# Performance work log

Measured on AMD Instinct MI355X. Metric: run time of the kernel, lower is better.

Reference implementation:

```python
import jax, jax.numpy as jnp
import numpy as np

NUM_EXPERT = 16
IN_FEAT = 1024
OUT_FEAT = 1024
BATCH = 8192


def setup_inputs() -> dict:
    key = jax.random.key(0)
    k_inp, k_gate, k_w = jax.random.split(key, 3)
    inp = jax.random.normal(k_inp, (BATCH, IN_FEAT), dtype=jnp.float32)
    gate = jax.random.randint(k_gate, (BATCH,), 0, NUM_EXPERT, dtype=jnp.int32)
    # nn.Linear default init: uniform(-1/sqrt(in_feat), 1/sqrt(in_feat))
    bound = 1.0 / np.sqrt(IN_FEAT)
    weight = jax.random.uniform(
        k_w, (NUM_EXPERT, OUT_FEAT, IN_FEAT), dtype=jnp.float32,
        minval=-bound, maxval=bound)
    return {"inp": inp, "gate": gate, "weight": weight}


def reference(inp, gate, weight):
    # o[t] = weight[gate[t]] @ inp[t]
    # Loop over the (small, fixed) expert axis via lax.scan; each step does a
    # dense [B, in] @ [in, out] GEMM and keeps rows routed to that expert.
    num_expert, out_feat, _ = weight.shape
    batch = inp.shape[0]

    def body(o, xs):
        i, w = xs  # w: [out_feat, in_feat]
        y = inp @ w.T  # [batch, out_feat]
        sel = (gate == i)[:, None]
        return jnp.where(sel, y, o), None

    o0 = jnp.zeros((batch, out_feat), dtype=inp.dtype)
    o, _ = jax.lax.scan(body, o0, (jnp.arange(num_expert), weight))
    return o
```

## Files before the change

kernel.cpp:

```cpp
#include <hip/hip_runtime.h>
#include <hip/hip_bf16.h>

#define NE    16
#define KDIM  1024
#define NDIM  1024
#define BATCH 8192
#define TM    128
#define TN    64
#define MAXT  96

typedef __attribute__((ext_vector_type(8))) short short8;
typedef __attribute__((ext_vector_type(4))) float floatx4;
typedef unsigned short ushort_t;

#define O_CNT  0
#define O_OFF  64
#define O_TG0  256
#define O_TE   1024
#define O_TEND 2048
#define O_POS  4096
#define O_TOK  36864
#define O_PA   73728
#define O_W    17113088
#define WS_REQ 50667520

#define GLOAD_LDS(gp, lp) __builtin_amdgcn_global_load_lds( \
    (const __attribute__((address_space(1))) unsigned int*)(gp), \
    (__attribute__((address_space(3))) unsigned int*)(lp), 16, 0, 0)

__device__ __forceinline__ unsigned int pk2bf(float x, float y) {
    __hip_bfloat162 h = __float22bfloat162_rn(make_float2(x, y));
    unsigned int u;
    __builtin_memcpy(&u, &h, 4);
    return u;
}


__global__ void zero_k(int* cnt) {
    if (threadIdx.x < NE) cnt[threadIdx.x] = 0;
}

__global__ void hist_k(const int* __restrict__ gate, int* cnt, int* pos) {
    int t = blockIdx.x * blockDim.x + threadIdx.x;
    if (t < BATCH) pos[t] = atomicAdd(&cnt[gate[t]], 1);
}

__global__ void scan_k(const int* __restrict__ cnt, int* off,
                       int* tg0, int* te, int* tend) {
    __shared__ int ntot;
    int t = threadIdx.x;
    if (t < NE) {
        int o = 0, ts = 0;
        for (int j = 0; j < NE; ++j) {
            int c = cnt[j];
            if (j < t) { o += c; ts += (c + TM - 1) / TM; }
        }
        int c = cnt[t];
        off[t] = o;
        if (t == NE - 1) { off[NE] = o + c; ntot = ts + (c + TM - 1) / TM; }
        int nt = ts;
        for (int r = 0; r < c; r += TM) {
            int r0 = (r + TM <= c) ? r : (c > TM ? c - TM : 0);
            tg0[nt] = o + r0; te[nt] = t; tend[nt] = o + c; ++nt;
        }
    }
    __syncthreads();
    for (int i = ntot + t; i < MAXT; i += 64) {
        tg0[i] = 0; te[i] = 0; tend[i] = 0;
    }
}

__global__ __launch_bounds__(256) void prep_k(
        const float* __restrict__ inp, const float* __restrict__ wgt,
        const int* __restrict__ gate, const int* __restrict__ pos,
        const int* __restrict__ off, ushort_t* __restrict__ pA,
        ushort_t* __restrict__ pW, int* __restrict__ tok) {
    int b = blockIdx.x, tid = threadIdx.x;
    if (b < BATCH) {
        int t = b;
        int g = off[gate[t]] + pos[t];
        float4 v = *(const float4*)&inp[(size_t)t * KDIM + tid * 4];
        uint2 u = make_uint2(pk2bf(v.x, v.y), pk2bf(v.z, v.w));
        *(uint2*)&pA[(size_t)g * KDIM + tid * 4] = u;
        if (tid == 0) tok[g] = t;
    } else {
        size_t i = (size_t)(b - BATCH) * 1024 + tid * 4;
        float4 v = *(const float4*)&wgt[i];
        uint2 u = make_uint2(pk2bf(v.x, v.y), pk2bf(v.z, v.w));
        *(uint2*)&pW[i] = u;
    }
}

__global__ __launch_bounds__(256, 4) void moe_gemm3_k(
        const ushort_t* __restrict__ pA, const ushort_t* __restrict__ pW,
        const int* __restrict__ tg0, const int* __restrict__ teArr,
        const int* __restrict__ tend, const int* __restrict__ tok,
        float* __restrict__ out) {
    const int y   = blockIdx.y;
    const int g0  = tg0[y];
    const int end = tend[y];
    if (g0 >= end) return;
    const int e    = teArr[y];
    const int out0 = blockIdx.x * TN;

    __shared__ ushort_t As[2][TM][32];
    __shared__ ushort_t Bs[2][TN][32];
    __shared__ int tok_s[TM];

    const int tid = threadIdx.x;
    if (tid < TM) tok_s[tid] = tok[g0 + tid];

    const int wave = tid >> 6, lane = tid & 63;
    const int wm = (wave >> 1) * 64;
    const int wn = (wave & 1) * 32;
    const int quad = lane >> 4, l16 = lane & 15;

    const ushort_t* Ab = pA + (size_t)g0 * KDIM;
    const ushort_t* Bb = pW + (size_t)e * (KDIM * NDIM) + (size_t)out0 * KDIM;

    floatx4 acc[4][2] = {};

    const int cA0 = wave * 64 + lane;
    const int cB  = wave * 64 + lane;

    {
        #pragma unroll
        for (int i = 0; i < 2; ++i) {
            int c = cA0 + i * 256;
            GLOAD_LDS(Ab + (c >> 2) * KDIM + (c & 3) * 8,
                      (ushort_t*)As[0] + (size_t)(i * 256 + wave * 64) * 8);
        }
        GLOAD_LDS(Bb + (cB >> 2) * KDIM + (cB & 3) * 8,
                  (ushort_t*)Bs[0] + (size_t)(wave * 64) * 8);
    }

    int buf = 0;
    for (int k0 = 0; k0 < KDIM; k0 += 32, buf ^= 1) {
        __syncthreads();
        if (k0 + 32 < KDIM) {
            int kn = k0 + 32;
            #pragma unroll
            for (int i = 0; i < 2; ++i) {
                int c = cA0 + i * 256;
                GLOAD_LDS(Ab + (c >> 2) * KDIM + kn + (c & 3) * 8,
                          (ushort_t*)As[buf ^ 1] + (size_t)(i * 256 + wave * 64) * 8);
            }
            GLOAD_LDS(Bb + (cB >> 2) * KDIM + kn + (cB & 3) * 8,
                      (ushort_t*)Bs[buf ^ 1] + (size_t)(wave * 64) * 8);
        }
        short8 a[4], b[2];
        #pragma unroll
        for (int i = 0; i < 4; ++i)
            a[i] = *(const short8*)&As[buf][wm + i * 16 + l16][quad * 8];
        #pragma unroll
        for (int i = 0; i < 2; ++i)
            b[i] = *(const short8*)&Bs[buf][wn + i * 16 + l16][quad * 8];
        #pragma unroll
        for (int mi = 0; mi < 4; ++mi)
            #pragma unroll
            for (int ni = 0; ni < 2; ++ni)
                acc[mi][ni] = __builtin_amdgcn_mfma_f32_16x16x32_bf16(
                    a[mi], b[ni], acc[mi][ni], 0, 0, 0);
    }

    #pragma unroll
    for (int mi = 0; mi < 4; ++mi) {
        #pragma unroll
        for (int r = 0; r < 4; ++r) {
            int lrow = wm + mi * 16 + quad * 4 + r;
            if (g0 + lrow < end) {
                int t = tok_s[lrow];
                float* orow = out + (size_t)t * NDIM + out0 + wn + l16;
                #pragma unroll
                for (int ni = 0; ni < 2; ++ni)
                    orow[ni * 16] = acc[mi][ni][r];
            }
        }
    }
}

#define LDW 20
__global__ void bin_tokens_k(const int* __restrict__ gate, int* cnt, int* idx) {
    int t = blockIdx.x * blockDim.x + threadIdx.x;
    if (t < BATCH) {
        int e = gate[t];
        int p = atomicAdd(&cnt[e], 1);
        idx[e * BATCH + p] = t;
    }
}

__global__ __launch_bounds__(256) void moe_gemm_k(
        const float* __restrict__ inp, const float* __restrict__ wgt,
        const int* __restrict__ cnt, const int* __restrict__ idx,
        float* __restrict__ out) {
    const int e = blockIdx.z;
    const int n_e = cnt[e];
    const int row0 = blockIdx.y * TM;
    if (row0 >= n_e) return;
    const int out0 = blockIdx.x * 128;
    __shared__ unsigned int As[TM * LDW];
    __shared__ unsigned int Bs[TM * LDW];
    __shared__ int tok_s[TM];
    const int tid = threadIdx.x;
    if (tid < TM) {
        int g = row0 + tid;
        tok_s[tid] = (g < n_e) ? idx[e * BATCH + g] : -1;
    }
    const int wave = tid >> 6, lane = tid & 63;
    const int wm = (wave >> 1) * 64, wn = (wave & 1) * 64;
    const int quad = lane >> 4, l16 = lane & 15;
    floatx4 acc[4][4] = {};
    const int cg = (tid & 7) * 4;
    const int rbase = tid >> 3;
    const float* wbase = wgt + (size_t)e * KDIM * NDIM;
    for (int k0 = 0; k0 < KDIM; k0 += 32) {
        __syncthreads();
        #pragma unroll
        for (int p = 0; p < 4; ++p) {
            int row = p * 32 + rbase;
            int t = tok_s[row];
            float4 va = make_float4(0.f, 0.f, 0.f, 0.f);
            if (t >= 0) va = *(const float4*)&inp[(size_t)t * KDIM + k0 + cg];
            As[row * LDW + (cg >> 1)]     = pk2bf(va.x, va.y);
            As[row * LDW + (cg >> 1) + 1] = pk2bf(va.z, va.w);
            float4 vb = *(const float4*)&wbase[(size_t)(out0 + row) * KDIM + k0 + cg];
            Bs[row * LDW + (cg >> 1)]     = pk2bf(vb.x, vb.y);
            Bs[row * LDW + (cg >> 1) + 1] = pk2bf(vb.z, vb.w);
        }
        __syncthreads();
        short8 a[4], b[4];
        #pragma unroll
        for (int i = 0; i < 4; ++i)
            a[i] = *(const short8*)&As[(wm + i * 16 + l16) * LDW + quad * 4];
        #pragma unroll
        for (int i = 0; i < 4; ++i)
            b[i] = *(const short8*)&Bs[(wn + i * 16 + l16) * LDW + quad * 4];
        #pragma unroll
        for (int mi = 0; mi < 4; ++mi)
            #pragma unroll
            for (int ni = 0; ni < 4; ++ni)
                acc[mi][ni] = __builtin_amdgcn_mfma_f32_16x16x32_bf16(
                    a[mi], b[ni], acc[mi][ni], 0, 0, 0);
    }
    #pragma unroll
    for (int mi = 0; mi < 4; ++mi) {
        #pragma unroll
        for (int r = 0; r < 4; ++r) {
            int lrow = wm + mi * 16 + quad * 4 + r;
            int t = tok_s[lrow];
            if (t >= 0) {
                float* orow = out + (size_t)t * NDIM + out0 + wn + l16;
                #pragma unroll
                for (int ni = 0; ni < 4; ++ni)
                    orow[ni * 16] = acc[mi][ni][r];
            }
        }
    }
}

extern "C" void kernel_launch(void* const* d_in, const int* in_sizes, int n_in,
                              void* d_out, int out_size, void* d_ws, size_t ws_size,
                              hipStream_t stream) {
    const float* inp  = (const float*)d_in[0];
    const int*   gate = (const int*)d_in[1];
    const float* wgt  = (const float*)d_in[2];
    float*       out  = (float*)d_out;
    char* w = (char*)d_ws;

    if (ws_size >= WS_REQ) {
        int* cnt  = (int*)(w + O_CNT);
        int* off  = (int*)(w + O_OFF);
        int* tg0  = (int*)(w + O_TG0);
        int* te   = (int*)(w + O_TE);
        int* tend = (int*)(w + O_TEND);
        int* pos  = (int*)(w + O_POS);
        int* tok  = (int*)(w + O_TOK);
        ushort_t* pA = (ushort_t*)(w + O_PA);
        ushort_t* pW = (ushort_t*)(w + O_W);

        zero_k<<<1, 64, 0, stream>>>(cnt);
        hist_k<<<BATCH / 256, 256, 0, stream>>>(gate, cnt, pos);
        scan_k<<<1, 64, 0, stream>>>(cnt, off, tg0, te, tend);
        prep_k<<<BATCH + NE * 1024, 256, 0, stream>>>(inp, wgt, gate, pos, off,
                                                      pA, pW, tok);
        dim3 grid(NDIM / TN, MAXT, 1);
        moe_gemm3_k<<<grid, 256, 0, stream>>>(pA, pW, tg0, te, tend, tok, out);
    } else {
        int* cnt = (int*)d_ws;
        int* idx = cnt + NE;
        zero_k<<<1, 64, 0, stream>>>(cnt);
        bin_tokens_k<<<BATCH / 256, 256, 0, stream>>>(gate, cnt, idx);
        dim3 grid(NDIM / 128, BATCH / TM, NE);
        moe_gemm_k<<<grid, 256, 0, stream>>>(inp, wgt, cnt, idx, out);
    }
}
```

Measured before the change: 199.8 us.

## Fold scan into prep kernel and use swizzled single-buffer K=64 GEMM tiles

Removes the separate scan kernel: each prep block computes its expert offset directly from the counts, and one extra block builds the tile tables. Weight conversion now handles 8 elements per thread with half as many blocks. The GEMM replaces the double-buffered K=32 LDS pipeline with a single-buffered K=64 tile that uses an XOR swizzle to avoid LDS bank conflicts. Occupancy is raised to 5 blocks per CU to hide the load latency that the lost prefetch overlap no longer covers. This trades explicit load/compute overlap for fewer barriers per K, conflict-free LDS reads and one fewer launch.

Result: faster. 194.1 us (-2.8%).

```diff
diff --git a/kernel.cpp b/kernel.cpp
--- a/kernel.cpp
+++ b/kernel.cpp
@@ -14,7 +14,6 @@
 typedef unsigned short ushort_t;
 
 #define O_CNT  0
-#define O_OFF  64
 #define O_TG0  256
 #define O_TE   1024
 #define O_TEND 2048
@@ -45,53 +44,53 @@
     if (t < BATCH) pos[t] = atomicAdd(&cnt[gate[t]], 1);
 }
 
-__global__ void scan_k(const int* __restrict__ cnt, int* off,
-                       int* tg0, int* te, int* tend) {
-    __shared__ int ntot;
-    int t = threadIdx.x;
-    if (t < NE) {
-        int o = 0, ts = 0;
-        for (int j = 0; j < NE; ++j) {
-            int c = cnt[j];
-            if (j < t) { o += c; ts += (c + TM - 1) / TM; }
-        }
-        int c = cnt[t];
-        off[t] = o;
-        if (t == NE - 1) { off[NE] = o + c; ntot = ts + (c + TM - 1) / TM; }
-        int nt = ts;
-        for (int r = 0; r < c; r += TM) {
-            int r0 = (r + TM <= c) ? r : (c > TM ? c - TM : 0);
-            tg0[nt] = o + r0; te[nt] = t; tend[nt] = o + c; ++nt;
-        }
-    }
-    __syncthreads();
-    for (int i = ntot + t; i < MAXT; i += 64) {
-        tg0[i] = 0; te[i] = 0; tend[i] = 0;
-    }
-}
-
 __global__ __launch_bounds__(256) void prep_k(
         const float* __restrict__ inp, const float* __restrict__ wgt,
         const int* __restrict__ gate, const int* __restrict__ pos,
-        const int* __restrict__ off, ushort_t* __restrict__ pA,
-        ushort_t* __restrict__ pW, int* __restrict__ tok) {
+        const int* __restrict__ cnt, ushort_t* __restrict__ pA,
+        ushort_t* __restrict__ pW, int* __restrict__ tok,
+        int* __restrict__ tg0, int* __restrict__ te, int* __restrict__ tend) {
+    __shared__ int ntot;
     int b = blockIdx.x, tid = threadIdx.x;
     if (b < BATCH) {
-        int t = b;
-        int g = off[gate[t]] + pos[t];
-        float4 v = *(const float4*)&inp[(size_t)t * KDIM + tid * 4];
+        int e = gate[b];
+        int off = 0;
+        #pragma unroll
+        for (int j = 0; j < NE; ++j) off += (j < e) ? cnt[j] : 0;
+        int g = off + pos[b];
+        float4 v = *(const float4*)&inp[(size_t)b * KDIM + tid * 4];
         uint2 u = make_uint2(pk2bf(v.x, v.y), pk2bf(v.z, v.w));
         *(uint2*)&pA[(size_t)g * KDIM + tid * 4] = u;
-        if (tid == 0) tok[g] = t;
+        if (tid == 0) tok[g] = b;
+    } else if (b < BATCH + 8192) {
+        size_t base = (size_t)(b - BATCH) * 2048 + tid * 8;
+        float4 v0 = *(const float4*)&wgt[base];
+        float4 v1 = *(const float4*)&wgt[base + 4];
+        *(uint2*)&pW[base]     = make_uint2(pk2bf(v0.x, v0.y), pk2bf(v0.z, v0.w));
+        *(uint2*)&pW[base + 4] = make_uint2(pk2bf(v1.x, v1.y), pk2bf(v1.z, v1.w));
     } else {
-        size_t i = (size_t)(b - BATCH) * 1024 + tid * 4;
-        float4 v = *(const float4*)&wgt[i];
-        uint2 u = make_uint2(pk2bf(v.x, v.y), pk2bf(v.z, v.w));
-        *(uint2*)&pW[i] = u;
-    }
-}
-
-__global__ __launch_bounds__(256, 4) void moe_gemm3_k(
+        if (tid < NE) {
+            int o = 0, ts = 0;
+            for (int j = 0; j < NE; ++j) {
+                int c = cnt[j];
+                if (j < tid) { o += c; ts += (c + TM - 1) / TM; }
+            }
+            int c = cnt[tid];
+            if (tid == NE - 1) ntot = ts + (c + TM - 1) / TM;
+            int nt = ts;
+            for (int r = 0; r < c; r += TM) {
+                int r0 = (r + TM <= c) ? r : (c > TM ? c - TM : 0);
+                tg0[nt] = o + r0; te[nt] = tid; tend[nt] = o + c; ++nt;
+            }
+        }
+        __syncthreads();
+        for (int i = ntot + tid; i < MAXT; i += 256) {
+            tg0[i] = 0; te[i] = 0; tend[i] = 0;
+        }
+    }
+}
+
+__global__ __launch_bounds__(256, 5) void moe_gemm4_k(
         const ushort_t* __restrict__ pA, const ushort_t* __restrict__ pW,
         const int* __restrict__ tg0, const int* __restrict__ teArr,
         const int* __restrict__ tend, const int* __restrict__ tok,
@@ -103,8 +102,8 @@
     const int e    = teArr[y];
     const int out0 = blockIdx.x * TN;
 
-    __shared__ ushort_t As[2][TM][32];
-    __shared__ ushort_t Bs[2][TN][32];
+    __shared__ ushort_t As[TM][64];
+    __shared__ ushort_t Bs[TN][64];
     __shared__ int tok_s[TM];
 
     const int tid = threadIdx.x;
@@ -119,48 +118,47 @@
     const ushort_t* Bb = pW + (size_t)e * (KDIM * NDIM) + (size_t)out0 * KDIM;
 
     floatx4 acc[4][2] = {};
-
-    const int cA0 = wave * 64 + lane;
-    const int cB  = wave * 64 + lane;
-
-    {
+    const int slotw = wave * 64 + lane;
+
+    for (int k0 = 0; k0 < KDIM; k0 += 64) {
+        #pragma unroll
+        for (int i = 0; i < 4; ++i) {
+            int slot = i * 256 + slotw;
+            int row = slot >> 3;
+            int kc = (slot & 7) ^ (row & 7);
+            GLOAD_LDS(Ab + (size_t)row * KDIM + k0 + kc * 8,
+                      (ushort_t*)As + (size_t)(i * 256 + wave * 64) * 8);
+        }
         #pragma unroll
         for (int i = 0; i < 2; ++i) {
-            int c = cA0 + i * 256;
-            GLOAD_LDS(Ab + (c >> 2) * KDIM + (c & 3) * 8,
-                      (ushort_t*)As[0] + (size_t)(i * 256 + wave * 64) * 8);
-        }
-        GLOAD_LDS(Bb + (cB >> 2) * KDIM + (cB & 3) * 8,
-                  (ushort_t*)Bs[0] + (size_t)(wave * 64) * 8);
-    }
-
-    int buf = 0;
-    for (int k0 = 0; k0 < KDIM; k0 += 32, buf ^= 1) {
-        __syncthreads();
-        if (k0 + 32 < KDIM) {
-            int kn = k0 + 32;
-            #pragma unroll
-            for (int i = 0; i < 2; ++i) {
-                int c = cA0 + i * 256;
-                GLOAD_LDS(Ab + (c >> 2) * KDIM + kn + (c & 3) * 8,
-                          (ushort_t*)As[buf ^ 1] + (size_t)(i * 256 + wave * 64) * 8);
-            }
-            GLOAD_LDS(Bb + (cB >> 2) * KDIM + kn + (cB & 3) * 8,
-                      (ushort_t*)Bs[buf ^ 1] + (size_t)(wave * 64) * 8);
-        }
-        short8 a[4], b[2];
-        #pragma unroll
-        for (int i = 0; i < 4; ++i)
-            a[i] = *(const short8*)&As[buf][wm + i * 16 + l16][quad * 8];
-        #pragma unroll
-        for (int i = 0; i < 2; ++i)
-            b[i] = *(const short8*)&Bs[buf][wn + i * 16 + l16][quad * 8];
-        #pragma unroll
-        for (int mi = 0; mi < 4; ++mi)
-            #pragma unroll
-            for (int ni = 0; ni < 2; ++ni)
-                acc[mi][ni] = __builtin_amdgcn_mfma_f32_16x16x32_bf16(
-                    a[mi], b[ni], acc[mi][ni], 0, 0, 0);
+            int slot = i * 256 + slotw;
+            int row = slot >> 3;
+            int kc = (slot & 7) ^ (row & 7);
+            GLOAD_LDS(Bb + (size_t)row * KDIM + k0 + kc * 8,
+                      (ushort_t*)Bs + (size_t)(i * 256 + wave * 64) * 8);
+        }
+        __syncthreads();
+        #pragma unroll
+        for (int s = 0; s < 2; ++s) {
+            short8 a[4], b[2];
+            #pragma unroll
+            for (int i = 0; i < 4; ++i) {
+                int r = wm + i * 16 + l16;
+                a[i] = *(const short8*)&As[r][((s * 4 + quad) ^ (r & 7)) * 8];
+            }
+            #pragma unroll
+            for (int j = 0; j < 2; ++j) {
+                int r = wn + j * 16 + l16;
+                b[j] = *(const short8*)&Bs[r][((s * 4 + quad) ^ (r & 7)) * 8];
+            }
+            #pragma unroll
+            for (int mi = 0; mi < 4; ++mi)
+                #pragma unroll
+                for (int nj = 0; nj < 2; ++nj)
+                    acc[mi][nj] = __builtin_amdgcn_mfma_f32_16x16x32_bf16(
+                        a[mi], b[nj], acc[mi][nj], 0, 0, 0);
+        }
+        __syncthreads();
     }
 
     #pragma unroll
@@ -172,8 +170,8 @@
                 int t = tok_s[lrow];
                 float* orow = out + (size_t)t * NDIM + out0 + wn + l16;
                 #pragma unroll
-                for (int ni = 0; ni < 2; ++ni)
-                    orow[ni * 16] = acc[mi][ni][r];
+                for (int nj = 0; nj < 2; ++nj)
+                    orow[nj * 16] = acc[mi][nj][r];
             }
         }
     }
@@ -269,7 +267,6 @@
 
     if (ws_size >= WS_REQ) {
         int* cnt  = (int*)(w + O_CNT);
-        int* off  = (int*)(w + O_OFF);
         int* tg0  = (int*)(w + O_TG0);
         int* te   = (int*)(w + O_TE);
         int* tend = (int*)(w + O_TEND);
@@ -280,11 +277,10 @@
 
         zero_k<<<1, 64, 0, stream>>>(cnt);
         hist_k<<<BATCH / 256, 256, 0, stream>>>(gate, cnt, pos);
-        scan_k<<<1, 64, 0, stream>>>(cnt, off, tg0, te, tend);
-        prep_k<<<BATCH + NE * 1024, 256, 0, stream>>>(inp, wgt, gate, pos, off,
-                                                      pA, pW, tok);
+        prep_k<<<BATCH + 8192 + 1, 256, 0, stream>>>(inp, wgt, gate, pos, cnt,
+                                                     pA, pW, tok, tg0, te, tend);
         dim3 grid(NDIM / TN, MAXT, 1);
-        moe_gemm3_k<<<grid, 256, 0, stream>>>(pA, pW, tg0, te, tend, tok, out);
+        moe_gemm4_k<<<grid, 256, 0, stream>>>(pA, pW, tg0, te, tend, tok, out);
     } else {
         int* cnt = (int*)d_ws;
         int* idx = cnt + NE;
```
